# Kernel tuning notes

Measured on AMD Instinct MI355X. Metric: run time of the kernel, lower is better.

Reference implementation:

```python
import jax, jax.numpy as jnp
import numpy as np

N, E, H, D_IN, L, G, T = 50000, 800000, 64, 64, 4, 128, 1

def _w(key, shape, fan_in):
    return jax.random.normal(key, shape, dtype=jnp.float32) / np.sqrt(fan_in)

def setup_inputs() -> dict:
    key = jax.random.key(0)
    ks = jax.random.split(key, 24)
    inp = {
        'x': jax.random.normal(ks[0], (N, D_IN), dtype=jnp.float32),
        'w': jax.random.normal(ks[1], (E, 1), dtype=jnp.float32),
        'src': jax.random.randint(ks[2], (E,), 0, N, dtype=jnp.int32),
        'dst': jax.random.randint(ks[3], (E,), 0, N, dtype=jnp.int32),
        'graph_id': jnp.sort(jax.random.randint(ks[4], (N,), 0, G, dtype=jnp.int32)),
        # input MLP (1 layer, last_activation None; SiLU applied in input_node_func)
        'W_in': _w(ks[5], (D_IN, H), D_IN), 'b_in': jnp.zeros((H,), jnp.float32),
        # per-layer message MLP: (2H+1 -> H -> H), SiLU mid and last
        'msg_W1': _w(ks[6], (L, 2 * H + 1, H), 2 * H + 1), 'msg_b1': jnp.zeros((L, H), jnp.float32),
        'msg_W2': _w(ks[7], (L, H, H), H), 'msg_b2': jnp.zeros((L, H), jnp.float32),
        # per-layer update MLP: (H -> H -> H), SiLU mid, last None
        'upd_W1': _w(ks[8], (L, H, H), H), 'upd_b1': jnp.zeros((L, H), jnp.float32),
        'upd_W2': _w(ks[9], (L, H, H), H), 'upd_b2': jnp.zeros((L, H), jnp.float32),
        # node-wise output MLP: (H -> H -> H), SiLU mid, last None
        'out_W1': _w(ks[10], (H, H), H), 'out_b1': jnp.zeros((H,), jnp.float32),
        'out_W2': _w(ks[11], (H, H), H), 'out_b2': jnp.zeros((H,), jnp.float32),
        # readout MLP: (3H -> H -> T), SiLU mid, last None
        'ro_W1': _w(ks[12], (3 * H, H), 3 * H), 'ro_b1': jnp.zeros((H,), jnp.float32),
        'ro_W2': _w(ks[13], (H, T), H), 'ro_b2': jnp.zeros((T,), jnp.float32),
    }
    return inp

def reference(x, w, src, dst, graph_id, W_in, b_in, msg_W1, msg_b1, msg_W2, msg_b2,
              upd_W1, upd_b1, upd_W2, upd_b2, out_W1, out_b1, out_W2, out_b2,
              ro_W1, ro_b1, ro_W2, ro_b2):
    silu = jax.nn.silu
    f = silu(x @ W_in + b_in)                                   # [N, H]
    sq = w * w                                                  # [E, 1]
    for l in range(L):
        mi = jnp.concatenate([f[src], f[dst], sq], axis=-1)     # [E, 2H+1]
        msg = silu(silu(mi @ msg_W1[l] + msg_b1[l]) @ msg_W2[l] + msg_b2[l])
        m = msg * jax.nn.sigmoid(msg)                           # gated message
        m_sum = jax.ops.segment_sum(m, dst, num_segments=N)     # scatter-sum to dst
        h_new = silu((m_sum + f) @ upd_W1[l] + upd_b1[l]) @ upd_W2[l] + upd_b2[l]
        f = h_new + f                                           # residual
    f = silu(f @ out_W1 + out_b1) @ out_W2 + out_b2             # node-wise output
    g_sum = jax.ops.segment_sum(f, graph_id, num_segments=G)
    cnt = jax.ops.segment_sum(jnp.ones((N, 1), f.dtype), graph_id, num_segments=G)
    g_mean = g_sum / jnp.maximum(cnt, 1.0)
    g_max = jax.ops.segment_max(f, graph_id, num_segments=G)
    readout = jnp.concatenate([g_sum, g_mean, g_max], axis=-1)  # [G, 3H]
    return silu(readout @ ro_W1 + ro_b1) @ ro_W2 + ro_b2        # [G, T]
```

## Files before the change

### kernel.cpp

```cpp
#include <hip/hip_runtime.h>

#define NN 50000
#define EE 800000
#define GG 128
#define LL 4
#define SCAN_B 196

typedef __bf16 bf16x8 __attribute__((ext_vector_type(8)));
typedef __bf16 bf16x4 __attribute__((ext_vector_type(4)));
typedef float  f32x4  __attribute__((ext_vector_type(4)));

__device__ __forceinline__ float silu_f(float x){
    float t = __builtin_amdgcn_exp2f(-1.44269504f * x);
    return x * __builtin_amdgcn_rcpf(1.0f + t);
}
__device__ __forceinline__ unsigned fenc(float v){
    unsigned u = __float_as_uint(v);
    return (u & 0x80000000u) ? ~u : (u | 0x80000000u);
}
__device__ __forceinline__ float fdec(unsigned u){
    return (u & 0x80000000u) ? __uint_as_float(u & 0x7fffffffu) : __uint_as_float(~u);
}

__global__ __launch_bounds__(256) void pack_k(
        const float* __restrict__ msgW1, const float* __restrict__ msgW2,
        const float* __restrict__ updW1, const float* __restrict__ updW2,
        const float* __restrict__ outW1, const float* __restrict__ outW2,
        const float* __restrict__ W_in, __bf16* __restrict__ pk){
    int m = blockIdx.x;
    const float* src;
    if(m<20){
        int l=m/5, r=m%5;
        if(r==0)      src = msgW1 + (size_t)l*129*64;
        else if(r==1) src = msgW1 + (size_t)l*129*64 + 64*64;
        else if(r==2) src = msgW2 + (size_t)l*64*64;
        else if(r==3) src = updW1 + (size_t)l*64*64;
        else          src = updW2 + (size_t)l*64*64;
    } else if(m==20) src=outW1; else if(m==21) src=outW2; else src=W_in;
    __bf16* dst = pk + (size_t)m*4096;
    int tid=threadIdx.x;
    #pragma unroll
    for(int i=0;i<16;++i){
        int idx = tid*16+i;
        int frag = idx>>9, lane=(idx>>3)&63, j=idx&7;
        int s=frag>>2, ng=frag&3, q=lane>>4, nn=lane&15;
        dst[idx] = (__bf16)src[(32*s+8*q+j)*64 + 16*ng + nn];
    }
}
__device__ __forceinline__ bf16x8 ldfrag(const __bf16* pk, int s, int ng, int lane){
    return *(const bf16x8*)&pk[(((s*4+ng)*64 + lane))*8];
}

__global__ __launch_bounds__(256) void input_mfma(const float* __restrict__ x,
        const __bf16* __restrict__ pkW, const float* __restrict__ bg,
        float* __restrict__ f, __bf16* __restrict__ f16, int N){
    int tid=threadIdx.x, wid=tid>>6, lane=tid&63;
    int q=lane>>4, nn=lane&15;
    bf16x8 Bf[2][4];
    #pragma unroll
    for(int s=0;s<2;++s)
        #pragma unroll
        for(int ng=0;ng<4;++ng) Bf[s][ng]=ldfrag(pkW,s,ng,lane);
    float bias[4];
    #pragma unroll
    for(int ng=0;ng<4;++ng) bias[ng]=bg[16*ng+nn];

    int ntiles=(N+15)/16;
    int gw=gridDim.x*4;
    for(int t=blockIdx.x*4+wid; t<ntiles; t+=gw){
        int m=t*16+nn; int mc=(m<N)?m:(N-1);
        float4 a0=*(const float4*)&x[(size_t)mc*64 + 8*q];
        float4 a1=*(const float4*)&x[(size_t)mc*64 + 8*q + 4];
        float4 a2=*(const float4*)&x[(size_t)mc*64 + 32 + 8*q];
        float4 a3=*(const float4*)&x[(size_t)mc*64 + 32 + 8*q + 4];
        bf16x8 af0, af1;
        af0[0]=(__bf16)a0.x; af0[1]=(__bf16)a0.y; af0[2]=(__bf16)a0.z; af0[3]=(__bf16)a0.w;
        af0[4]=(__bf16)a1.x; af0[5]=(__bf16)a1.y; af0[6]=(__bf16)a1.z; af0[7]=(__bf16)a1.w;
        af1[0]=(__bf16)a2.x; af1[1]=(__bf16)a2.y; af1[2]=(__bf16)a2.z; af1[3]=(__bf16)a2.w;
        af1[4]=(__bf16)a3.x; af1[5]=(__bf16)a3.y; af1[6]=(__bf16)a3.z; af1[7]=(__bf16)a3.w;
        #pragma unroll
        for(int ng=0;ng<4;++ng){
            f32x4 acc; acc[0]=bias[ng]; acc[1]=bias[ng]; acc[2]=bias[ng]; acc[3]=bias[ng];
            acc=__builtin_amdgcn_mfma_f32_16x16x32_bf16(af0,Bf[0][ng],acc,0,0,0);
            acc=__builtin_amdgcn_mfma_f32_16x16x32_bf16(af1,Bf[1][ng],acc,0,0,0);
            #pragma unroll
            for(int r=0;r<4;++r){
                int row=t*16+4*q+r;
                if(row<N){
                    float o=silu_f(acc[r]);
                    f[(size_t)row*64+16*ng+nn]=o;
                    f16[(size_t)row*64+16*ng+nn]=(__bf16)o;
                }
            }
        }
    }
}

__global__ void hist_k(const int* __restrict__ dst, int* __restrict__ deg, int E){
    int e=blockIdx.x*blockDim.x+threadIdx.x;
    if(e<E) atomicAdd(&deg[dst[e]],1);
}

__global__ __launch_bounds__(256) void scan1_k(const int* __restrict__ deg, int* __restrict__ curs,
        int* __restrict__ bsum, int N){
    __shared__ int sv[256];
    int tid=threadIdx.x;
    int idx=blockIdx.x*256+tid;
    int v=(idx<N)?deg[idx]:0;
    sv[tid]=v; __syncthreads();
    #pragma unroll
    for(int off=1; off<256; off<<=1){
        int a=(tid>=off)?sv[tid-off]:0;
        __syncthreads(); sv[tid]+=a; __syncthreads();
    }
    if(idx<N) curs[idx]=sv[tid]-v;
    if(tid==255) bsum[blockIdx.x]=sv[255];
}
__global__ __launch_bounds__(256) void scan2_k(int* __restrict__ bsum, int B){
    __shared__ int sv[256];
    int tid=threadIdx.x;
    int v=(tid<B)?bsum[tid]:0;
    sv[tid]=v; __syncthreads();
    #pragma unroll
    for(int off=1; off<256; off<<=1){
        int a=(tid>=off)?sv[tid-off]:0;
        __syncthreads(); sv[tid]+=a; __syncthreads();
    }
    if(tid<B) bsum[tid]=sv[tid]-v;
}
__global__ __launch_bounds__(256) void scan3_k(int* __restrict__ curs, const int* __restrict__ bsum, int N){
    int idx=blockIdx.x*256+threadIdx.x;
    if(idx<N) curs[idx]+=bsum[blockIdx.x];
}

__global__ void fill_k(const int* __restrict__ src, const int* __restrict__ dst,
                       const float* __restrict__ w, int* __restrict__ cursor,
                       int4* __restrict__ meta, int E){
    int e=blockIdx.x*blockDim.x+threadIdx.x;
    if(e<E){
        int d=dst[e];
        int r=atomicAdd(&cursor[d],1);
        float ww=w[e];
        int4 v; v.x=src[e]; v.y=d; v.z=__float_as_int(ww*ww); v.w=0;
        meta[r]=v;
    }
}

__global__ __launch_bounds__(256) void xy_mfma(const __bf16* __restrict__ f16,
        const __bf16* __restrict__ pkA, const __bf16* __restrict__ pkB,
        const float* __restrict__ b1, __bf16* __restrict__ XY, int N){
    int tid=threadIdx.x, wid=tid>>6, lane=tid&63;
    int q=lane>>4, nn=lane&15;
    bf16x8 Bf[2][8];
    #pragma unroll
    for(int s=0;s<2;++s){
        #pragma unroll
        for(int ng=0;ng<4;++ng){ Bf[s][ng]=ldfrag(pkA,s,ng,lane); Bf[s][4+ng]=ldfrag(pkB,s,ng,lane); }
    }
    float bias[8];
    #pragma unroll
    for(int ng=0;ng<8;++ng) bias[ng]=(ng<4)?0.f:b1[16*(ng-4)+nn];
    int ntiles=(N+15)/16;
    int gw=gridDim.x*4;
    for(int t=blockIdx.x*4+wid; t<ntiles; t+=gw){
        int row=t*16+nn; if(row>=N) row=N-1;
        bf16x8 a0=*(const bf16x8*)&f16[(size_t)row*64 + 8*q];
        bf16x8 a1=*(const bf16x8*)&f16[(size_t)row*64 + 32 + 8*q];
        #pragma unroll
        for(int ng=0;ng<8;++ng){
            f32x4 acc; acc[0]=bias[ng]; acc[1]=bias[ng]; acc[2]=bias[ng]; acc[3]=bias[ng];
            acc=__builtin_amdgcn_mfma_f32_16x16x32_bf16(a0,Bf[0][ng],acc,0,0,0);
            acc=__builtin_amdgcn_mfma_f32_16x16x32_bf16(a1,Bf[1][ng],acc,0,0,0);
            #pragma unroll
            for(int r=0;r<4;++r){
                int orow=t*16+4*q+r;
                if(orow<N) XY[(size_t)orow*128 + 16*ng + nn]=(__bf16)acc[r];
            }
        }
    }
}

__global__ __launch_bounds__(256) void edge_mfma6(
        const __bf16* __restrict__ XY, const int4* __restrict__ meta,
        const __bf16* __restrict__ pkW2,
        const float* __restrict__ W1, const float* __restrict__ b2,
        float* __restrict__ msum, int E){
    int tid=threadIdx.x, wid=tid>>6, lane=tid&63;
    int q=lane>>4, nn=lane&15;

    bf16x8 B2f[2][4];
    #pragma unroll
    for(int s=0;s<2;++s)
        #pragma unroll
        for(int ng=0;ng<4;++ng) B2f[s][ng]=ldfrag(pkW2,s,ng,lane);
    float w128lo[8], w128hi[8];
    #pragma unroll
    for(int j=0;j<8;++j){
        w128lo[j]=W1[128*64 + 8*q+j];
        w128hi[j]=W1[128*64 + 32+8*q+j];
    }
    float bias2[4];
    #pragma unroll
    for(int ng=0;ng<4;++ng) bias2[ng]=b2[16*ng+nn];

    __shared__ __align__(16) __bf16 sm16[4][32][68];
    int cpos = 4*(lane&15) + (lane>>4);

    int ntiles=E/32;
    int nw=gridDim.x*4;
    int chunk=(ntiles+nw-1)/nw;
    int wgl=blockIdx.x*4+wid;
    int t0=wgl*chunk, t1=t0+chunk; if(t1>ntiles) t1=ntiles;
    if(t0>=t1) return;

    int4 mv  = meta[(size_t)t0*32 + (lane&31)];
    int4 mvn = (t0+1<t1) ? meta[(size_t)(t0+1)*32 + (lane&31)] : mv;
    bf16x8 gx0lo,gx0hi,gy0lo,gy0hi,gx1lo,gx1hi,gy1lo,gy1hi;
    {
        int se0=__shfl(mv.x, nn,64),    de0=__shfl(mv.y, nn,64);
        int se1=__shfl(mv.x, 16+nn,64), de1=__shfl(mv.y, 16+nn,64);
        const __bf16* xp0=XY+(size_t)se0*128; const __bf16* yp0=XY+(size_t)de0*128+64;
        const __bf16* xp1=XY+(size_t)se1*128; const __bf16* yp1=XY+(size_t)de1*128+64;
        gx0lo=*(const bf16x8*)(xp0+8*q); gx0hi=*(const bf16x8*)(xp0+32+8*q);
        gy0lo=*(const bf16x8*)(yp0+8*q); gy0hi=*(const bf16x8*)(yp0+32+8*q);
        gx1lo=*(const bf16x8*)(xp1+8*q); gx1hi=*(const bf16x8*)(xp1+32+8*q);
        gy1lo=*(const bf16x8*)(yp1+8*q); gy1hi=*(const bf16x8*)(yp1+32+8*q);
    }
    int cur=__builtin_amdgcn_readlane(mv.y, 0);
    float vsum=0.f;

    for(int t=t0;t<t1;++t){
        int4 mv2 = mvn;
        if(t+2<t1) mv2 = meta[(size_t)(t+2)*32 + (lane&31)];

        int d_ = mv.y;
        float w2v = __int_as_float(mv.z);

        bf16x8 A0lo,A0hi,A1lo,A1hi;
        {
            float w2a = __shfl(w2v, nn, 64);
            float w2b = __shfl(w2v, 16+nn, 64);
            #pragma unroll
            for(int j=0;j<8;++j){
                A0lo[j]=(__bf16)silu_f((float)gx0lo[j] + (float)gy0lo[j] + w2a*w128lo[j]);
                A0hi[j]=(__bf16)silu_f((float)gx0hi[j] + (float)gy0hi[j] + w2a*w128hi[j]);
                A1lo[j]=(__bf16)silu_f((float)gx1lo[j] + (float)gy1lo[j] + w2b*w128lo[j]);
                A1hi[j]=(__bf16)silu_f((float)gx1hi[j] + (float)gy1hi[j] + w2b*w128hi[j]);
            }
        }
        if(t+1<t1){
            int se0=__shfl(mvn.x, nn,64),    de0=__shfl(mvn.y, nn,64);
            int se1=__shfl(mvn.x, 16+nn,64), de1=__shfl(mvn.y, 16+nn,64);
            const __bf16* xp0=XY+(size_t)se0*128; const __bf16* yp0=XY+(size_t)de0*128+64;
            const __bf16* xp1=XY+(size_t)se1*128; const __bf16* yp1=XY+(size_t)de1*128+64;
            gx0lo=*(const bf16x8*)(xp0+8*q); gx0hi=*(const bf16x8*)(xp0+32+8*q);
            gy0lo=*(const bf16x8*)(yp0+8*q); gy0hi=*(const bf16x8*)(yp0+32+8*q);
            gx1lo=*(const bf16x8*)(xp1+8*q); gx1hi=*(const bf16x8*)(xp1+32+8*q);
            gy1lo=*(const bf16x8*)(yp1+8*q); gy1hi=*(const bf16x8*)(yp1+32+8*q);
        }
        #pragma unroll
        for(int h=0;h<2;++h){
            bf16x8 alo = h ? A1lo : A0lo;
            bf16x8 ahi = h ? A1hi : A0hi;
            f32x4 acc2[4];
            #pragma unroll
            for(int ng=0;ng<4;++ng){ f32x4 c; c[0]=bias2[ng]; c[1]=bias2[ng]; c[2]=bias2[ng]; c[3]=bias2[ng]; acc2[ng]=c; }
            #pragma unroll
            for(int ng=0;ng<4;++ng){
                acc2[ng]=__builtin_amdgcn_mfma_f32_16x16x32_bf16(alo,B2f[0][ng],acc2[ng],0,0,0);
                acc2[ng]=__builtin_amdgcn_mfma_f32_16x16x32_bf16(ahi,B2f[1][ng],acc2[ng],0,0,0);
            }
            #pragma unroll
            for(int r=0;r<4;++r){
                bf16x4 pv;
                #pragma unroll
                for(int ng=0;ng<4;++ng) pv[ng]=(__bf16)silu_f(silu_f(acc2[ng][r]));
                *(bf16x4*)&sm16[wid][16*h+4*q+r][4*nn] = pv;
            }
        }
        asm volatile("" ::: "memory");
        {
            int dprev = __shfl(d_, (lane+63)&63, 64);
            unsigned long long bal = __ballot(lane>=1 && lane<32 && d_!=dprev);
            unsigned bmask = (unsigned)bal;
            int d0 = __builtin_amdgcn_readlane(d_, 0);
            if(d0 != cur) bmask |= 1u;
            #pragma unroll
            for(int r=0;r<32;++r){
                if(bmask & (1u<<r)){
                    atomicAdd(&msum[(size_t)cur*64+lane], vsum);
                    vsum=0.f;
                    cur=__builtin_amdgcn_readlane(d_, r);
                }
                vsum += (float)sm16[wid][r][cpos];
            }
        }
        asm volatile("" ::: "memory");
        mv = mvn; mvn = mv2;
    }
    atomicAdd(&msum[(size_t)cur*64+lane], vsum);
}

__global__ __launch_bounds__(256) void node_mfma(float* A, const float* F,
        const __bf16* __restrict__ pkW1, const float* __restrict__ b1,
        const __bf16* __restrict__ pkW2, const float* __restrict__ b2,
        float* __restrict__ out, __bf16* __restrict__ out16, int zeroA,
        const __bf16* __restrict__ pkXYa, const __bf16* __restrict__ pkXYb,
        const float* __restrict__ bXY, __bf16* __restrict__ XYout, int N){
    int tid=threadIdx.x, wid=tid>>6, lane=tid&63;
    int q=lane>>4, nn=lane&15;

    bf16x8 B1f[2][4], B2f[2][4];
    #pragma unroll
    for(int s=0;s<2;++s)
        #pragma unroll
        for(int ng=0;ng<4;++ng){ B1f[s][ng]=ldfrag(pkW1,s,ng,lane); B2f[s][ng]=ldfrag(pkW2,s,ng,lane); }
    float bias1[4], bias2[4];
    #pragma unroll
    for(int ng=0;ng<4;++ng){ bias1[ng]=b1[16*ng+nn]; bias2[ng]=b2[16*ng+nn]; }
    bool hasXY = (pkXYa != nullptr);
    float bXYv[4];
    #pragma unroll
    for(int j=0;j<4;++j) bXYv[j] = hasXY ? bXY[16*j+nn] : 0.f;

    __shared__ __align__(16) __bf16 sh1[4][16][72];
    __shared__ __align__(16) float sF[4][16][68];
    bool hasF = (F != nullptr);

    int ntiles=(N+15)/16;
    int gw=gridDim.x*4;
    for(int t=blockIdx.x*4+wid; t<ntiles; t+=gw){
        int m=t*16+nn;
        int mc=(m<N)?m:(N-1);
        float4 a0=*(const float4*)&A[(size_t)mc*64 + 8*q];
        float4 a1=*(const float4*)&A[(size_t)mc*64 + 8*q + 4];
        float4 a2=*(const float4*)&A[(size_t)mc*64 + 32 + 8*q];
        float4 a3=*(const float4*)&A[(size_t)mc*64 + 32 + 8*q + 4];
        if(hasF){
            float4 f0=*(const float4*)&F[(size_t)mc*64 + 8*q];
            float4 f1=*(const float4*)&F[(size_t)mc*64 + 8*q + 4];
            float4 f2_=*(const float4*)&F[(size_t)mc*64 + 32 + 8*q];
            float4 f3=*(const float4*)&F[(size_t)mc*64 + 32 + 8*q + 4];
            a0.x+=f0.x; a0.y+=f0.y; a0.z+=f0.z; a0.w+=f0.w;
            a1.x+=f1.x; a1.y+=f1.y; a1.z+=f1.z; a1.w+=f1.w;
            a2.x+=f2_.x; a2.y+=f2_.y; a2.z+=f2_.z; a2.w+=f2_.w;
            a3.x+=f3.x; a3.y+=f3.y; a3.z+=f3.z; a3.w+=f3.w;
            *(float4*)&sF[wid][nn][8*q]   = f0;
            *(float4*)&sF[wid][nn][8*q+4] = f1;
            *(float4*)&sF[wid][nn][32+8*q]   = f2_;
            *(float4*)&sF[wid][nn][32+8*q+4] = f3;
        }
        if(zeroA && m<N){
            float4 z; z.x=0.f; z.y=0.f; z.z=0.f; z.w=0.f;
            *(float4*)&A[(size_t)mc*64 + 8*q]      = z;
            *(float4*)&A[(size_t)mc*64 + 8*q + 4]  = z;
            *(float4*)&A[(size_t)mc*64 + 32 + 8*q] = z;
            *(float4*)&A[(size_t)mc*64 + 32 + 8*q + 4] = z;
        }
        bf16x8 af0, af1;
        af0[0]=(__bf16)a0.x; af0[1]=(__bf16)a0.y; af0[2]=(__bf16)a0.z; af0[3]=(__bf16)a0.w;
        af0[4]=(__bf16)a1.x; af0[5]=(__bf16)a1.y; af0[6]=(__bf16)a1.z; af0[7]=(__bf16)a1.w;
        af1[0]=(__bf16)a2.x; af1[1]=(__bf16)a2.y; af1[2]=(__bf16)a2.z; af1[3]=(__bf16)a2.w;
        af1[4]=(__bf16)a3.x; af1[5]=(__bf16)a3.y; af1[6]=(__bf16)a3.z; af1[7]=(__bf16)a3.w;

        f32x4 acc[4];
        #pragma unroll
        for(int ng=0;ng<4;++ng){ f32x4 c; c[0]=bias1[ng]; c[1]=bias1[ng]; c[2]=bias1[ng]; c[3]=bias1[ng]; acc[ng]=c; }
        #pragma unroll
        for(int ng=0;ng<4;++ng){
            acc[ng]=__builtin_amdgcn_mfma_f32_16x16x32_bf16(af0,B1f[0][ng],acc[ng],0,0,0);
            acc[ng]=__builtin_amdgcn_mfma_f32_16x16x32_bf16(af1,B1f[1][ng],acc[ng],0,0,0);
        }
        #pragma unroll
        for(int ng=0;ng<4;++ng)
            #pragma unroll
            for(int r=0;r<4;++r)
                sh1[wid][4*q+r][16*ng+nn]=(__bf16)silu_f(acc[ng][r]);
        asm volatile("" ::: "memory");
        bf16x8 a20=*(const bf16x8*)&sh1[wid][nn][8*q];
        bf16x8 a21=*(const bf16x8*)&sh1[wid][nn][32+8*q];
        f32x4 acc2[4];
        #pragma unroll
        for(int ng=0;ng<4;++ng){ f32x4 c; c[0]=bias2[ng]; c[1]=bias2[ng]; c[2]=bias2[ng]; c[3]=bias2[ng]; acc2[ng]=c; }
        #pragma unroll
        for(int ng=0;ng<4;++ng){
            acc2[ng]=__builtin_amdgcn_mfma_f32_16x16x32_bf16(a20,B2f[0][ng],acc2[ng],0,0,0);
            acc2[ng]=__builtin_amdgcn_mfma_f32_16x16x32_bf16(a21,B2f[1][ng],acc2[ng],0,0,0);
        }
        #pragma unroll
        for(int ng=0;ng<4;++ng)
            #pragma unroll
            for(int r=0;r<4;++r){
                int row=t*16+4*q+r;
                float o=acc2[ng][r];
                if(hasF) o += sF[wid][4*q+r][16*ng+nn];
                if(row<N){
                    out[(size_t)row*64 + 16*ng + nn]=o;
                    if(out16) out16[(size_t)row*64 + 16*ng + nn]=(__bf16)o;
                }
                if(hasXY) sh1[wid][4*q+r][16*ng+nn]=(__bf16)o;
            }
        asm volatile("" ::: "memory");
        if(hasXY){
            bf16x8 a30=*(const bf16x8*)&sh1[wid][nn][8*q];
            bf16x8 a31=*(const bf16x8*)&sh1[wid][nn][32+8*q];
            #pragma unroll
            for(int ng=0;ng<8;++ng){
                const __bf16* pkx = (ng<4)? pkXYa : pkXYb;
                int g2 = ng&3;
                float bb = (ng<4)?0.f:bXYv[ng-4];
                f32x4 accx; accx[0]=bb; accx[1]=bb; accx[2]=bb; accx[3]=bb;
                accx=__builtin_amdgcn_mfma_f32_16x16x32_bf16(a30,ldfrag(pkx,0,g2,lane),accx,0,0,0);
                accx=__builtin_amdgcn_mfma_f32_16x16x32_bf16(a31,ldfrag(pkx,1,g2,lane),accx,0,0,0);
                #pragma unroll
                for(int r=0;r<4;++r){
                    int row=t*16+4*q+r;
                    if(row<N) XYout[(size_t)row*128 + 16*ng + nn]=(__bf16)accx[r];
                }
            }
        }
        asm volatile("" ::: "memory");
    }
}

__global__ __launch_bounds__(256) void seg_reduce_sorted(const float* __restrict__ f2, const int* __restrict__ gid,
        float* __restrict__ gsum, unsigned* __restrict__ gmaxu, float* __restrict__ cnt, int N){
    int wgl=blockIdx.x*4 + (threadIdx.x>>6);
    int lane=threadIdx.x&63;
    int W=gridDim.x*4;
    int chunk=(N+W-1)/W;
    int n0=wgl*chunk;
    int n1=n0+chunk; if(n1>N) n1=N;
    if(n0>=n1) return;
    int cur=gid[n0];
    float s=0.f, mx=-__builtin_inff(), c=0.f;
    for(int n=n0;n<n1;++n){
        int g=gid[n];
        float v=f2[(size_t)n*64+lane];
        if(g!=cur){
            atomicAdd(&gsum[(size_t)cur*64+lane], s);
            atomicMax(&gmaxu[(size_t)cur*64+lane], fenc(mx));
            if(lane==0) atomicAdd(&cnt[cur], c);
            s=0.f; mx=-__builtin_inff(); c=0.f; cur=g;
        }
        s+=v; mx=fmaxf(mx,v); c+=1.f;
    }
    atomicAdd(&gsum[(size_t)cur*64+lane], s);
    atomicMax(&gmaxu[(size_t)cur*64+lane], fenc(mx));
    if(lane==0) atomicAdd(&cnt[cur], c);
}

__global__ __launch_bounds__(256) void readout_k(const float* __restrict__ gsum, const unsigned* __restrict__ gmaxu,
        const float* __restrict__ cnt,
        const float* __restrict__ W1, const float* __restrict__ b1,
        const float* __restrict__ W2, const float* __restrict__ b2,
        float* __restrict__ out, int G){
    __shared__ __align__(16) float sr[4][192];
    int tid=threadIdx.x, wid=tid>>6, lane=tid&63;
    int g=blockIdx.x*4+wid;
    if(g<G){
        float s_=gsum[g*64+lane];
        float c=cnt[g];
        float mean=s_/fmaxf(c,1.0f);
        float mx=fdec(gmaxu[g*64+lane]);
        sr[wid][lane]=s_; sr[wid][64+lane]=mean; sr[wid][128+lane]=mx;
    }
    __syncthreads();
    if(g<G){
        float h=b1[lane];
        for(int k=0;k<192;k+=4){
            float4 r4=*(const float4*)&sr[wid][k];
            h += r4.x*W1[(k+0)*64+lane] + r4.y*W1[(k+1)*64+lane]
               + r4.z*W1[(k+2)*64+lane] + r4.w*W1[(k+3)*64+lane];
        }
        h=silu_f(h);
        float p=h*W2[lane];
        #pragma unroll
        for(int off=32;off>0;off>>=1) p += __shfl_down(p, off, 64);
        if(lane==0) out[g]=p+b2[0];
    }
}

extern "C" void kernel_launch(void* const* d_in, const int* in_sizes, int n_in,
                              void* d_out, int out_size, void* d_ws, size_t ws_size,
                              hipStream_t stream){
    const float* x     = (const float*)d_in[0];
    const float* w     = (const float*)d_in[1];
    const int*   src   = (const int*)d_in[2];
    const int*   dst   = (const int*)d_in[3];
    const int*   gid   = (const int*)d_in[4];
    const float* W_in  = (const float*)d_in[5];
    const float* b_in  = (const float*)d_in[6];
    const float* msgW1 = (const float*)d_in[7];
    const float* msgb1 = (const float*)d_in[8];
    const float* msgW2 = (const float*)d_in[9];
    const float* msgb2 = (const float*)d_in[10];
    const float* updW1 = (const float*)d_in[11];
    const float* updb1 = (const float*)d_in[12];
    const float* updW2 = (const float*)d_in[13];
    const float* updb2 = (const float*)d_in[14];
    const float* outW1 = (const float*)d_in[15];
    const float* outb1 = (const float*)d_in[16];
    const float* outW2 = (const float*)d_in[17];
    const float* outb2 = (const float*)d_in[18];
    const float* roW1  = (const float*)d_in[19];
    const float* rob1  = (const float*)d_in[20];
    const float* roW2  = (const float*)d_in[21];
    const float* rob2  = (const float*)d_in[22];

    float*  f     = (float*)d_ws;
    float*  msum  = f + (size_t)NN*64;
    float*  f2    = msum;
    __bf16* f16   = (__bf16*)(msum + (size_t)NN*64);
    __bf16* XY    = f16 + (size_t)NN*64;
    int4*   meta  = (int4*)(XY + (size_t)NN*128);
    __bf16* pk    = (__bf16*)(meta + EE);
    int*    deg   = (int*)(pk + 23*4096);
    int*    curs  = deg + 50048;
    int*    bsum  = curs + 50048;
    float*  gsum  = (float*)(bsum + 256);
    unsigned* gmaxu = (unsigned*)(gsum + GG*64);
    float*  cnt   = (float*)(gmaxu + GG*64);

    pack_k<<<dim3(23),dim3(256),0,stream>>>(msgW1, msgW2, updW1, updW2, outW1, outW2, W_in, pk);

    hipMemsetAsync(deg, 0, 50048*sizeof(int), stream);
    hist_k<<<dim3((EE+255)/256),dim3(256),0,stream>>>(dst, deg, EE);
    scan1_k<<<dim3(SCAN_B),dim3(256),0,stream>>>(deg, curs, bsum, NN);
    scan2_k<<<dim3(1),dim3(256),0,stream>>>(bsum, SCAN_B);
    scan3_k<<<dim3(SCAN_B),dim3(256),0,stream>>>(curs, bsum, NN);
    fill_k<<<dim3((EE+255)/256),dim3(256),0,stream>>>(src, dst, w, curs, meta, EE);

    hipMemsetAsync(msum, 0, (size_t)NN*64*sizeof(float), stream);
    input_mfma<<<dim3(782),dim3(256),0,stream>>>(x, pk + (size_t)22*4096, b_in, f, f16, NN);
    xy_mfma<<<dim3(512),dim3(256),0,stream>>>(f16,
        pk + (size_t)0*4096, pk + (size_t)1*4096, msgb1 + 0*64, XY, NN);
    for(int l=0;l<LL;++l){
        edge_mfma6<<<dim3(1280),dim3(256),0,stream>>>(XY, meta,
            pk + (size_t)(5*l+2)*4096,
            msgW1 + (size_t)l*129*64, msgb2 + l*64, msum, EE);
        bool fuse = (l < LL-1);
        node_mfma<<<dim3(782),dim3(256),0,stream>>>(msum, f,
            pk + (size_t)(5*l+3)*4096, updb1 + l*64,
            pk + (size_t)(5*l+4)*4096, updb2 + l*64, f, nullptr, 1,
            fuse ? pk + (size_t)(5*(l+1)+0)*4096 : nullptr,
            fuse ? pk + (size_t)(5*(l+1)+1)*4096 : nullptr,
            fuse ? msgb1 + (l+1)*64 : nullptr,
            XY, NN);
    }
    node_mfma<<<dim3(782),dim3(256),0,stream>>>(f, nullptr,
        pk + (size_t)20*4096, outb1, pk + (size_t)21*4096, outb2, f2, nullptr, 0,
        nullptr, nullptr, nullptr, nullptr, NN);
    hipMemsetAsync(gsum, 0, (size_t)(GG*64*2 + GG)*sizeof(float), stream);
    seg_reduce_sorted<<<dim3(256),dim3(256),0,stream>>>(f2, gid, gsum, gmaxu, cnt, NN);
    readout_k<<<dim3(32),dim3(256),0,stream>>>(gsum, gmaxu, cnt, roW1, rob1, roW2, rob2, (float*)d_out, GG);
}
```

Baseline: 542.3 us.

## Fuse first-layer XY projection into input kernel and fuse graph pooling into readout

The input MLP kernel now stages its SiLU output through LDS and computes the layer-0 XY projection directly, which removes the separate xy_mfma launch and the bf16 f16 buffer round trip. The segmented sum/max/count kernel with atomics, its memset, and the separate readout kernel are replaced by one readout kernel. In that kernel each wave binary-searches its graph's node range in the sorted graph_id and reduces it directly. The cost is that only 128 waves (32 blocks) now read all 50000x64 node features, so the pooling step has much less parallelism. The input kernel also reloads weight fragments from global memory inside its tile loop.

```diff
diff --git a/kernel.cpp b/kernel.cpp
--- a/kernel.cpp
+++ b/kernel.cpp
@@ -13,13 +13,6 @@
 __device__ __forceinline__ float silu_f(float x){
     float t = __builtin_amdgcn_exp2f(-1.44269504f * x);
     return x * __builtin_amdgcn_rcpf(1.0f + t);
-}
-__device__ __forceinline__ unsigned fenc(float v){
-    unsigned u = __float_as_uint(v);
-    return (u & 0x80000000u) ? ~u : (u | 0x80000000u);
-}
-__device__ __forceinline__ float fdec(unsigned u){
-    return (u & 0x80000000u) ? __uint_as_float(u & 0x7fffffffu) : __uint_as_float(~u);
 }
 
 __global__ __launch_bounds__(256) void pack_k(
@@ -53,7 +46,9 @@
 
 __global__ __launch_bounds__(256) void input_mfma(const float* __restrict__ x,
         const __bf16* __restrict__ pkW, const float* __restrict__ bg,
-        float* __restrict__ f, __bf16* __restrict__ f16, int N){
+        const __bf16* __restrict__ pkXYa, const __bf16* __restrict__ pkXYb,
+        const float* __restrict__ bXY,
+        float* __restrict__ f, __bf16* __restrict__ XYout, int N){
     int tid=threadIdx.x, wid=tid>>6, lane=tid&63;
     int q=lane>>4, nn=lane&15;
     bf16x8 Bf[2][4];
@@ -61,9 +56,11 @@
     for(int s=0;s<2;++s)
         #pragma unroll
         for(int ng=0;ng<4;++ng) Bf[s][ng]=ldfrag(pkW,s,ng,lane);
-    float bias[4];
-    #pragma unroll
-    for(int ng=0;ng<4;++ng) bias[ng]=bg[16*ng+nn];
+    float bias[4], bXYv[4];
+    #pragma unroll
+    for(int ng=0;ng<4;++ng){ bias[ng]=bg[16*ng+nn]; bXYv[ng]=bXY[16*ng+nn]; }
+
+    __shared__ __align__(16) __bf16 sh1[4][16][72];
 
     int ntiles=(N+15)/16;
     int gw=gridDim.x*4;
@@ -86,13 +83,29 @@
             #pragma unroll
             for(int r=0;r<4;++r){
                 int row=t*16+4*q+r;
-                if(row<N){
-                    float o=silu_f(acc[r]);
-                    f[(size_t)row*64+16*ng+nn]=o;
-                    f16[(size_t)row*64+16*ng+nn]=(__bf16)o;
-                }
-            }
-        }
+                float o=silu_f(acc[r]);
+                if(row<N) f[(size_t)row*64+16*ng+nn]=o;
+                sh1[wid][4*q+r][16*ng+nn]=(__bf16)o;
+            }
+        }
+        asm volatile("" ::: "memory");
+        bf16x8 a30=*(const bf16x8*)&sh1[wid][nn][8*q];
+        bf16x8 a31=*(const bf16x8*)&sh1[wid][nn][32+8*q];
+        #pragma unroll
+        for(int ng=0;ng<8;++ng){
+            const __bf16* pkx = (ng<4)? pkXYa : pkXYb;
+            int g2 = ng&3;
+            float bb = (ng<4)?0.f:bXYv[ng-4];
+            f32x4 accx; accx[0]=bb; accx[1]=bb; accx[2]=bb; accx[3]=bb;
+            accx=__builtin_amdgcn_mfma_f32_16x16x32_bf16(a30,ldfrag(pkx,0,g2,lane),accx,0,0,0);
+            accx=__builtin_amdgcn_mfma_f32_16x16x32_bf16(a31,ldfrag(pkx,1,g2,lane),accx,0,0,0);
+            #pragma unroll
+            for(int r=0;r<4;++r){
+                int row=t*16+4*q+r;
+                if(row<N) XYout[(size_t)row*128 + 16*ng + nn]=(__bf16)accx[r];
+            }
+        }
+        asm volatile("" ::: "memory");
     }
 }
 
@@ -143,40 +156,6 @@
         float ww=w[e];
         int4 v; v.x=src[e]; v.y=d; v.z=__float_as_int(ww*ww); v.w=0;
         meta[r]=v;
-    }
-}
-
-__global__ __launch_bounds__(256) void xy_mfma(const __bf16* __restrict__ f16,
-        const __bf16* __restrict__ pkA, const __bf16* __restrict__ pkB,
-        const float* __restrict__ b1, __bf16* __restrict__ XY, int N){
-    int tid=threadIdx.x, wid=tid>>6, lane=tid&63;
-    int q=lane>>4, nn=lane&15;
-    bf16x8 Bf[2][8];
-    #pragma unroll
-    for(int s=0;s<2;++s){
-        #pragma unroll
-        for(int ng=0;ng<4;++ng){ Bf[s][ng]=ldfrag(pkA,s,ng,lane); Bf[s][4+ng]=ldfrag(pkB,s,ng,lane); }
-    }
-    float bias[8];
-    #pragma unroll
-    for(int ng=0;ng<8;++ng) bias[ng]=(ng<4)?0.f:b1[16*(ng-4)+nn];
-    int ntiles=(N+15)/16;
-    int gw=gridDim.x*4;
-    for(int t=blockIdx.x*4+wid; t<ntiles; t+=gw){
-        int row=t*16+nn; if(row>=N) row=N-1;
-        bf16x8 a0=*(const bf16x8*)&f16[(size_t)row*64 + 8*q];
-        bf16x8 a1=*(const bf16x8*)&f16[(size_t)row*64 + 32 + 8*q];
-        #pragma unroll
-        for(int ng=0;ng<8;++ng){
-            f32x4 acc; acc[0]=bias[ng]; acc[1]=bias[ng]; acc[2]=bias[ng]; acc[3]=bias[ng];
-            acc=__builtin_amdgcn_mfma_f32_16x16x32_bf16(a0,Bf[0][ng],acc,0,0,0);
-            acc=__builtin_amdgcn_mfma_f32_16x16x32_bf16(a1,Bf[1][ng],acc,0,0,0);
-            #pragma unroll
-            for(int r=0;r<4;++r){
-                int orow=t*16+4*q+r;
-                if(orow<N) XY[(size_t)orow*128 + 16*ng + nn]=(__bf16)acc[r];
-            }
-        }
     }
 }
 
@@ -304,7 +283,7 @@
 __global__ __launch_bounds__(256) void node_mfma(float* A, const float* F,
         const __bf16* __restrict__ pkW1, const float* __restrict__ b1,
         const __bf16* __restrict__ pkW2, const float* __restrict__ b2,
-        float* __restrict__ out, __bf16* __restrict__ out16, int zeroA,
+        float* __restrict__ out, int zeroA,
         const __bf16* __restrict__ pkXYa, const __bf16* __restrict__ pkXYb,
         const float* __restrict__ bXY, __bf16* __restrict__ XYout, int N){
     int tid=threadIdx.x, wid=tid>>6, lane=tid&63;
@@ -394,10 +373,7 @@
                 int row=t*16+4*q+r;
                 float o=acc2[ng][r];
                 if(hasF) o += sF[wid][4*q+r][16*ng+nn];
-                if(row<N){
-                    out[(size_t)row*64 + 16*ng + nn]=o;
-                    if(out16) out16[(size_t)row*64 + 16*ng + nn]=(__bf16)o;
-                }
+                if(row<N) out[(size_t)row*64 + 16*ng + nn]=o;
                 if(hasXY) sh1[wid][4*q+r][16*ng+nn]=(__bf16)o;
             }
         asm volatile("" ::: "memory");
@@ -423,47 +399,34 @@
     }
 }
 
-__global__ __launch_bounds__(256) void seg_reduce_sorted(const float* __restrict__ f2, const int* __restrict__ gid,
-        float* __restrict__ gsum, unsigned* __restrict__ gmaxu, float* __restrict__ cnt, int N){
-    int wgl=blockIdx.x*4 + (threadIdx.x>>6);
-    int lane=threadIdx.x&63;
-    int W=gridDim.x*4;
-    int chunk=(N+W-1)/W;
-    int n0=wgl*chunk;
-    int n1=n0+chunk; if(n1>N) n1=N;
-    if(n0>=n1) return;
-    int cur=gid[n0];
-    float s=0.f, mx=-__builtin_inff(), c=0.f;
-    for(int n=n0;n<n1;++n){
-        int g=gid[n];
-        float v=f2[(size_t)n*64+lane];
-        if(g!=cur){
-            atomicAdd(&gsum[(size_t)cur*64+lane], s);
-            atomicMax(&gmaxu[(size_t)cur*64+lane], fenc(mx));
-            if(lane==0) atomicAdd(&cnt[cur], c);
-            s=0.f; mx=-__builtin_inff(); c=0.f; cur=g;
-        }
-        s+=v; mx=fmaxf(mx,v); c+=1.f;
-    }
-    atomicAdd(&gsum[(size_t)cur*64+lane], s);
-    atomicMax(&gmaxu[(size_t)cur*64+lane], fenc(mx));
-    if(lane==0) atomicAdd(&cnt[cur], c);
-}
-
-__global__ __launch_bounds__(256) void readout_k(const float* __restrict__ gsum, const unsigned* __restrict__ gmaxu,
-        const float* __restrict__ cnt,
+__global__ __launch_bounds__(256) void readout_fused(const float* __restrict__ f2,
+        const int* __restrict__ gid,
         const float* __restrict__ W1, const float* __restrict__ b1,
         const float* __restrict__ W2, const float* __restrict__ b2,
-        float* __restrict__ out, int G){
+        float* __restrict__ out, int N, int G){
     __shared__ __align__(16) float sr[4][192];
     int tid=threadIdx.x, wid=tid>>6, lane=tid&63;
     int g=blockIdx.x*4+wid;
     if(g<G){
-        float s_=gsum[g*64+lane];
-        float c=cnt[g];
-        float mean=s_/fmaxf(c,1.0f);
-        float mx=fdec(gmaxu[g*64+lane]);
-        sr[wid][lane]=s_; sr[wid][64+lane]=mean; sr[wid][128+lane]=mx;
+        int lo=0, hi=N;
+        while(lo<hi){ int mid=(lo+hi)>>1; if(gid[mid]<g) lo=mid+1; else hi=mid; }
+        int a=lo, b=N;
+        while(a<b){ int mid=(a+b)>>1; if(gid[mid]<g+1) a=mid+1; else b=mid; }
+        int n0=lo, n1=a;
+        float s=0.f, mx=-__builtin_inff();
+        int n=n0;
+        for(; n+4<=n1; n+=4){
+            float v0=f2[(size_t)(n+0)*64+lane];
+            float v1=f2[(size_t)(n+1)*64+lane];
+            float v2=f2[(size_t)(n+2)*64+lane];
+            float v3=f2[(size_t)(n+3)*64+lane];
+            s += (v0+v1)+(v2+v3);
+            mx = fmaxf(mx, fmaxf(fmaxf(v0,v1), fmaxf(v2,v3)));
+        }
+        for(; n<n1; ++n){ float v=f2[(size_t)n*64+lane]; s+=v; mx=fmaxf(mx,v); }
+        float c=(float)(n1-n0);
+        float mean=s/fmaxf(c,1.0f);
+        sr[wid][lane]=s; sr[wid][64+lane]=mean; sr[wid][128+lane]=mx;
     }
     __syncthreads();
     if(g<G){
@@ -511,16 +474,12 @@
     float*  f     = (float*)d_ws;
     float*  msum  = f + (size_t)NN*64;
     float*  f2    = msum;
-    __bf16* f16   = (__bf16*)(msum + (size_t)NN*64);
-    __bf16* XY    = f16 + (size_t)NN*64;
+    __bf16* XY    = (__bf16*)(msum + (size_t)NN*64);
     int4*   meta  = (int4*)(XY + (size_t)NN*128);
     __bf16* pk    = (__bf16*)(meta + EE);
     int*    deg   = (int*)(pk + 23*4096);
     int*    curs  = deg + 50048;
     int*    bsum  = curs + 50048;
-    float*  gsum  = (float*)(bsum + 256);
-    unsigned* gmaxu = (unsigned*)(gsum + GG*64);
-    float*  cnt   = (float*)(gmaxu + GG*64);
 
     pack_k<<<dim3(23),dim3(256),0,stream>>>(msgW1, msgW2, updW1, updW2, outW1, outW2, W_in, pk);
 
@@ -532,9 +491,8 @@
     fill_k<<<dim3((EE+255)/256),dim3(256),0,stream>>>(src, dst, w, curs, meta, EE);
 
     hipMemsetAsync(msum, 0, (size_t)NN*64*sizeof(float), stream);
-    input_mfma<<<dim3(782),dim3(256),0,stream>>>(x, pk + (size_t)22*4096, b_in, f, f16, NN);
-    xy_mfma<<<dim3(512),dim3(256),0,stream>>>(f16,
-        pk + (size_t)0*4096, pk + (size_t)1*4096, msgb1 + 0*64, XY, NN);
+    input_mfma<<<dim3(782),dim3(256),0,stream>>>(x, pk + (size_t)22*4096, b_in,
+        pk + (size_t)0*4096, pk + (size_t)1*4096, msgb1 + 0*64, f, XY, NN);
     for(int l=0;l<LL;++l){
         edge_mfma6<<<dim3(1280),dim3(256),0,stream>>>(XY, meta,
             pk + (size_t)(5*l+2)*4096,
@@ -542,16 +500,15 @@
         bool fuse = (l < LL-1);
         node_mfma<<<dim3(782),dim3(256),0,stream>>>(msum, f,
             pk + (size_t)(5*l+3)*4096, updb1 + l*64,
-            pk + (size_t)(5*l+4)*4096, updb2 + l*64, f, nullptr, 1,
+            pk + (size_t)(5*l+4)*4096, updb2 + l*64, f, 1,
             fuse ? pk + (size_t)(5*(l+1)+0)*4096 : nullptr,
             fuse ? pk + (size_t)(5*(l+1)+1)*4096 : nullptr,
             fuse ? msgb1 + (l+1)*64 : nullptr,
             XY, NN);
     }
     node_mfma<<<dim3(782),dim3(256),0,stream>>>(f, nullptr,
-        pk + (size_t)20*4096, outb1, pk + (size_t)21*4096, outb2, f2, nullptr, 0,
+        pk + (size_t)20*4096, outb1, pk + (size_t)21*4096, outb2, f2, 0,
         nullptr, nullptr, nullptr, nullptr, NN);
-    hipMemsetAsync(gsum, 0, (size_t)(GG*64*2 + GG)*sizeof(float), stream);
-    seg_reduce_sorted<<<dim3(256),dim3(256),0,stream>>>(f2, gid, gsum, gmaxu, cnt, NN);
-    readout_k<<<dim3(32),dim3(256),0,stream>>>(gsum, gmaxu, cnt, roW1, rob1, roW2, rob2, (float*)d_out, GG);
-}
+    readout_fused<<<dim3(32),dim3(256),0,stream>>>(f2, gid, roW1, rob1, roW2, rob2,
+        (float*)d_out, NN, GG);
+}
```

Result: slower. 562.7 us (+3.8%).
